# Performance work log

Hardware: AMD Instinct MI355X
Metric: run time of the kernel (lower is better)

The kernel has to match this reference:

```python
import jax, jax.numpy as jnp
import numpy as np

B, DIM_IN, T = 16, 512, 2048
DIM_OUT2 = 512 * 2  # dim_out * 2 (GLU halves it)
K = 3
STYLE = 128
SCALE_CONV = 1.0 / np.sqrt(DIM_IN * K ** 2).astype(np.float32)  # fan_in = dim_in * k^2 (as in source)
SCALE_LIN = 1.0 / np.sqrt(STYLE).astype(np.float32)


def setup_inputs() -> dict:
    key = jax.random.key(0)
    ks = jax.random.split(key, 6)
    x = jax.random.normal(ks[0], (B, DIM_IN, T), dtype=jnp.float32)
    c_src = jax.random.normal(ks[1], (B, STYLE), dtype=jnp.float32)
    c_trg = jax.random.normal(ks[2], (B, STYLE), dtype=jnp.float32)
    # EqualLinear params (lr_mul=1): weight ~ N(0,1), bias filled with bias_init=1
    w_s = jax.random.normal(ks[3], (DIM_IN, STYLE), dtype=jnp.float32)
    b_s = jnp.ones((DIM_IN,), dtype=jnp.float32)
    w_b = jax.random.normal(ks[4], (DIM_IN, STYLE), dtype=jnp.float32)
    b_b = jnp.ones((DIM_IN,), dtype=jnp.float32)
    weight = jax.random.normal(ks[5], (1, DIM_OUT2, DIM_IN, K), dtype=jnp.float32)
    return {"x": x, "c_src": c_src, "c_trg": c_trg,
            "w_s": w_s, "b_s": b_s, "w_b": w_b, "b_b": b_b, "weight": weight}


def reference(x, c_src, c_trg, w_s, b_s, w_b, b_b, weight):
    bsz, cin, t = x.shape
    cout = weight.shape[1]  # dim_out * 2
    k = weight.shape[3]
    # EqualLinear: F.linear(c, w*scale, bias)
    s = (c_trg @ (w_s * SCALE_LIN).T + b_s).reshape(bsz, 1, cin, 1)
    beta = (c_trg @ (w_b * SCALE_LIN).T + b_b).reshape(bsz, 1, cin, 1)
    w = SCALE_CONV * (weight * s + beta)               # [B, Cout, Cin, K]
    demod = jax.lax.rsqrt(jnp.sum(w * w, axis=(2, 3)) + 1e-8)   # [B, Cout]
    demod_mean = jnp.mean(w.reshape(bsz, cout, -1), axis=2)      # [B, Cout]
    w = (w - demod_mean[:, :, None, None]) * demod[:, :, None, None]
    # batch-as-groups conv1d
    w = w.reshape(bsz * cout, cin, k)
    xr = x.reshape(1, bsz * cin, t)
    out = jax.lax.conv_general_dilated(
        xr, w, window_strides=(1,), padding=[(k // 2, k // 2)],
        dimension_numbers=("NCH", "OIH", "NCH"), feature_group_count=bsz)
    out = out.reshape(bsz, cout, -1)
    a, g = jnp.split(out, 2, axis=1)  # GLU on channel dim
    return a * jax.nn.sigmoid(g)
```

## Files before the change

### kernel.cpp

```cpp
#include <hip/hip_runtime.h>
#include <math.h>

typedef __attribute__((ext_vector_type(8))) short short8;
typedef __attribute__((ext_vector_type(4))) float f32x4;
typedef unsigned short ushortT;

#define NB     16
#define CIN    512
#define TT     2048
#define COUT2  1024
#define NSTYLE 128
#define KKTOT  1536
#define TPAD   2050
#define NKT    24

#define SCALE_LIN  0.088388347648318447f
#define SCALE_CONV 0.014731391274719736f

__device__ __forceinline__ ushortT f2bf(float f) {
  union { float f; unsigned u; } v; v.f = f;
  unsigned r = v.u + 0x7fffu + ((v.u >> 16) & 1u);
  return (ushortT)(r >> 16);
}

__device__ __forceinline__ void gload16(const void* g, void* l) {
  __builtin_amdgcn_global_load_lds(
      (const __attribute__((address_space(1))) void*)g,
      (__attribute__((address_space(3))) void*)l, 16, 0, 0);
}

__global__ void style_kernel(const float* __restrict__ c_trg,
                             const float* __restrict__ w_s, const float* __restrict__ b_s,
                             const float* __restrict__ w_b, const float* __restrict__ b_b,
                             float* __restrict__ s, float* __restrict__ beta,
                             ushortT* __restrict__ xT) {
  int gid = blockIdx.x * 256 + threadIdx.x;
  int b = gid >> 9, ci = gid & 511;
  const float* ct = c_trg + b * NSTYLE;
  const float* ws = w_s + ci * NSTYLE;
  const float* wb = w_b + ci * NSTYLE;
  float as = 0.f, ab = 0.f;
#pragma unroll 8
  for (int j = 0; j < NSTYLE; ++j) {
    float c = ct[j];
    as += c * ws[j];
    ab += c * wb[j];
  }
  s[gid]    = as * SCALE_LIN + b_s[ci];
  beta[gid] = ab * SCALE_LIN + b_b[ci];
  xT[(size_t)b * TPAD * CIN + ci] = 0;
  xT[((size_t)b * TPAD + TPAD - 1) * CIN + ci] = 0;
}

__global__ void xpose_kernel(const float* __restrict__ x, ushortT* __restrict__ xT) {
  int b = blockIdx.z, ct = blockIdx.y, tt = blockIdx.x;
  int t0 = tt * 64, ci0 = ct * 64;
  __shared__ float tile[64][65];
  const float* xB = x + (size_t)b * CIN * TT;
  int rr = threadIdx.x >> 4;
  int c4 = threadIdx.x & 15;
#pragma unroll
  for (int it = 0; it < 4; ++it) {
    int ci = rr + it * 16;
    float4 v = *(const float4*)(xB + (size_t)(ci0 + ci) * TT + t0 + c4 * 4);
    tile[ci][c4 * 4 + 0] = v.x; tile[ci][c4 * 4 + 1] = v.y;
    tile[ci][c4 * 4 + 2] = v.z; tile[ci][c4 * 4 + 3] = v.w;
  }
  __syncthreads();
  ushortT* xTB = xT + (size_t)b * TPAD * CIN;
#pragma unroll
  for (int it = 0; it < 4; ++it) {
    int t = rr + it * 16;
    ushort4 o;
    o.x = f2bf(tile[c4 * 4 + 0][t]); o.y = f2bf(tile[c4 * 4 + 1][t]);
    o.z = f2bf(tile[c4 * 4 + 2][t]); o.w = f2bf(tile[c4 * 4 + 3][t]);
    *(ushort4*)(xTB + (size_t)(1 + t0 + t) * CIN + ci0 + c4 * 4) = o;
  }
}

__global__ void modw_kernel(const float* __restrict__ weight,
                            const float* __restrict__ s, const float* __restrict__ beta,
                            ushortT* __restrict__ wnorm) {
  int co = blockIdx.x, tid = threadIdx.x;
  int ci = tid * 2;
  const float* wp = weight + (size_t)co * KKTOT + (size_t)ci * 3;
  float2 va = *(const float2*)(wp);
  float2 vb = *(const float2*)(wp + 2);
  float2 vc = *(const float2*)(wp + 4);
  float v0 = va.x, v1 = va.y, v2 = vb.x, v3 = vb.y, v4 = vc.x, v5 = vc.y;
  int r = ((co & 511) << 1) | (co >> 9);
  __shared__ float rs[4], rq[4];
  for (int b = 0; b < NB; ++b) {
    float2 sv = *(const float2*)(s + b * CIN + ci);
    float2 ev = *(const float2*)(beta + b * CIN + ci);
    float w0 = SCALE_CONV * (v0 * sv.x + ev.x);
    float w1 = SCALE_CONV * (v1 * sv.x + ev.x);
    float w2 = SCALE_CONV * (v2 * sv.x + ev.x);
    float w3 = SCALE_CONV * (v3 * sv.y + ev.y);
    float w4 = SCALE_CONV * (v4 * sv.y + ev.y);
    float w5 = SCALE_CONV * (v5 * sv.y + ev.y);
    float sum = w0 + w1 + w2 + w3 + w4 + w5;
    float sq  = w0*w0 + w1*w1 + w2*w2 + w3*w3 + w4*w4 + w5*w5;
#pragma unroll
    for (int off = 32; off; off >>= 1) {
      sum += __shfl_xor(sum, off);
      sq  += __shfl_xor(sq,  off);
    }
    if ((tid & 63) == 0) { rs[tid >> 6] = sum; rq[tid >> 6] = sq; }
    __syncthreads();
    float mean  = (rs[0] + rs[1] + rs[2] + rs[3]) * (1.0f / 1536.0f);
    float demod = rsqrtf(rq[0] + rq[1] + rq[2] + rq[3] + 1e-8f);
    ushortT* dst = wnorm + ((size_t)b * COUT2 + r) * KKTOT;
    ushort2 p0, p1, p2;
    p0.x = f2bf((w0 - mean) * demod); p0.y = f2bf((w3 - mean) * demod);
    p1.x = f2bf((w1 - mean) * demod); p1.y = f2bf((w4 - mean) * demod);
    p2.x = f2bf((w2 - mean) * demod); p2.y = f2bf((w5 - mean) * demod);
    *(ushort2*)(dst +        ci) = p0;
    *(ushort2*)(dst +  512 + ci) = p1;
    *(ushort2*)(dst + 1024 + ci) = p2;
    __syncthreads();
  }
}


#define AFRAG(d, s, f) (*(const short8*)(ldsc + ((d) * 4 + (s)) * 16384 + aoff + (f) * 1024))
#define BFRAG(d, s, g) (*(const short8*)(ldsc + ((d) * 4 + 2 + (s)) * 16384 + boff + (g) * 1024))

#define RDA(as_, d, s, mh) do {              \
    as_##0 = AFRAG(d, s, (mh) * 4 + 0);      \
    as_##1 = AFRAG(d, s, (mh) * 4 + 1);      \
    as_##2 = AFRAG(d, s, (mh) * 4 + 2);      \
    as_##3 = AFRAG(d, s, (mh) * 4 + 3);      \
  } while (0)

#define RDB(bs_, d, s) do {                  \
    bs_##0 = BFRAG(d, s, 0);                 \
    bs_##1 = BFRAG(d, s, 1);                 \
    bs_##2 = BFRAG(d, s, 2);                 \
    bs_##3 = BFRAG(d, s, 3);                 \
  } while (0)

#define STAGE_A(d, s, kt) do {                                                   \
    int kc_ = (kt) * 64 + (s) * 32;                                              \
    gload16(wB + (size_t)(co0 + r0) * KKTOT + kc_ + jbs8,                        \
            ldsw + ((d) * 4 + (s)) * 8192 + tid * 8);                            \
    gload16(wB + (size_t)(co0 + r0 + 128) * KKTOT + kc_ + jbs8,                  \
            ldsw + ((d) * 4 + (s)) * 8192 + 4096 + tid * 8);                     \
  } while (0)

#define STAGE_B(d, s, kt) do {                                                   \
    int kc_ = (kt) * 64 + (s) * 32;                                              \
    int tap_ = kc_ >> 9; int ci_ = kc_ & 511;                                    \
    gload16(xB + (size_t)(t0 + r0 + tap_) * CIN + ci_ + jbs8,                    \
            ldsw + ((d) * 4 + 2 + (s)) * 8192 + tid * 8);                        \
    gload16(xB + (size_t)(t0 + r0 + 128 + tap_) * CIN + ci_ + jbs8,              \
            ldsw + ((d) * 4 + 2 + (s)) * 8192 + 4096 + tid * 8);                 \
  } while (0)

#define PHASE(mh, au_, bu_, RD_CODE, STAGES, VMN) do {                           \
    if ((VMN) == 6)      asm volatile("s_waitcnt vmcnt(6)" ::: "memory");        \
    else if ((VMN) == 4) asm volatile("s_waitcnt vmcnt(4)" ::: "memory");        \
    else if ((VMN) == 0) asm volatile("s_waitcnt vmcnt(0)" ::: "memory");        \
    __builtin_amdgcn_s_barrier();                                                \
    RD_CODE;                                                                     \
    STAGES;                                                                      \
    __builtin_amdgcn_s_setprio(1);                                               \
    acc[(mh)*4+0][0] = __builtin_amdgcn_mfma_f32_16x16x32_bf16(au_##0, bu_##0, acc[(mh)*4+0][0], 0, 0, 0); \
    acc[(mh)*4+0][1] = __builtin_amdgcn_mfma_f32_16x16x32_bf16(au_##0, bu_##1, acc[(mh)*4+0][1], 0, 0, 0); \
    acc[(mh)*4+0][2] = __builtin_amdgcn_mfma_f32_16x16x32_bf16(au_##0, bu_##2, acc[(mh)*4+0][2], 0, 0, 0); \
    acc[(mh)*4+0][3] = __builtin_amdgcn_mfma_f32_16x16x32_bf16(au_##0, bu_##3, acc[(mh)*4+0][3], 0, 0, 0); \
    acc[(mh)*4+1][0] = __builtin_amdgcn_mfma_f32_16x16x32_bf16(au_##1, bu_##0, acc[(mh)*4+1][0], 0, 0, 0); \
    acc[(mh)*4+1][1] = __builtin_amdgcn_mfma_f32_16x16x32_bf16(au_##1, bu_##1, acc[(mh)*4+1][1], 0, 0, 0); \
    acc[(mh)*4+1][2] = __builtin_amdgcn_mfma_f32_16x16x32_bf16(au_##1, bu_##2, acc[(mh)*4+1][2], 0, 0, 0); \
    acc[(mh)*4+1][3] = __builtin_amdgcn_mfma_f32_16x16x32_bf16(au_##1, bu_##3, acc[(mh)*4+1][3], 0, 0, 0); \
    acc[(mh)*4+2][0] = __builtin_amdgcn_mfma_f32_16x16x32_bf16(au_##2, bu_##0, acc[(mh)*4+2][0], 0, 0, 0); \
    acc[(mh)*4+2][1] = __builtin_amdgcn_mfma_f32_16x16x32_bf16(au_##2, bu_##1, acc[(mh)*4+2][1], 0, 0, 0); \
    acc[(mh)*4+2][2] = __builtin_amdgcn_mfma_f32_16x16x32_bf16(au_##2, bu_##2, acc[(mh)*4+2][2], 0, 0, 0); \
    acc[(mh)*4+2][3] = __builtin_amdgcn_mfma_f32_16x16x32_bf16(au_##2, bu_##3, acc[(mh)*4+2][3], 0, 0, 0); \
    acc[(mh)*4+3][0] = __builtin_amdgcn_mfma_f32_16x16x32_bf16(au_##3, bu_##0, acc[(mh)*4+3][0], 0, 0, 0); \
    acc[(mh)*4+3][1] = __builtin_amdgcn_mfma_f32_16x16x32_bf16(au_##3, bu_##1, acc[(mh)*4+3][1], 0, 0, 0); \
    acc[(mh)*4+3][2] = __builtin_amdgcn_mfma_f32_16x16x32_bf16(au_##3, bu_##2, acc[(mh)*4+3][2], 0, 0, 0); \
    acc[(mh)*4+3][3] = __builtin_amdgcn_mfma_f32_16x16x32_bf16(au_##3, bu_##3, acc[(mh)*4+3][3], 0, 0, 0); \
    __builtin_amdgcn_s_setprio(0);                                               \
  } while (0)

__global__ __launch_bounds__(512, 2)
void conv_gemm8(const ushortT* __restrict__ wnorm, const ushortT* __restrict__ xT,
                float* __restrict__ out) {
  extern __shared__ ushortT ldsw[];
  const char* ldsc = (const char*)ldsw;

  int orig = blockIdx.x;
  int wgid = (orig & 7) * 64 + (orig >> 3);
  int b  = wgid >> 5;
  int i5 = wgid & 31;
  int mp = i5 >> 4, r2 = i5 & 15;
  int nt = r2 >> 1, mt = mp * 2 + (r2 & 1);
  int co0 = mt * 256, t0 = nt * 256;

  int tid = threadIdx.x;
  int l = tid & 63, w = tid >> 6;
  int wm = w & 1, wn = w >> 1;

  int r0 = tid >> 2;
  int jbs8 = (((tid & 3) ^ ((r0 >> 1) & 3)) << 3);
  int cb = ((l >> 4) ^ ((l >> 1) & 3));
  int aoff = (wm * 128 + (l & 15)) * 64 + cb * 16;
  int boff = (wn * 64  + (l & 15)) * 64 + cb * 16;

  const ushortT* wB = wnorm + (size_t)b * COUT2 * KKTOT;
  const ushortT* xB = xT + (size_t)b * TPAD * CIN;

  f32x4 acc[8][4];
#pragma unroll
  for (int i = 0; i < 8; ++i)
#pragma unroll
    for (int j = 0; j < 4; ++j)
      acc[i][j] = (f32x4){0.f, 0.f, 0.f, 0.f};
  short8 ax0 = {}, ax1 = {}, ax2 = {}, ax3 = {};
  short8 ay0 = {}, ay1 = {}, ay2 = {}, ay3 = {};
  short8 bx0 = {}, bx1 = {}, bx2 = {}, bx3 = {};
  short8 by0 = {}, by1 = {}, by2 = {}, by3 = {};

  STAGE_A(0, 0, 0); STAGE_B(0, 0, 0); STAGE_A(0, 1, 0); STAGE_B(0, 1, 0);
  STAGE_B(1, 0, 1); STAGE_A(1, 0, 1); STAGE_B(1, 1, 1);
  asm volatile("s_waitcnt vmcnt(6)" ::: "memory");
  __builtin_amdgcn_s_barrier();
  RDA(ax, 0, 0, 0);
  RDB(bx, 0, 0);

  for (int j = 0; j < 11; ++j) {
    int kt1 = 2 * j + 1;
    int k0n = 2 * j + 2, k1n = 2 * j + 3;
    PHASE(0, ax, bx, { RDA(ay, 0, 0, 1); },                  STAGE_A(1, 1, kt1), -1);
    PHASE(1, ay, bx, { RDA(ax, 0, 1, 0); RDB(by, 0, 1); },   STAGE_B(0, 0, k0n), -1);
    PHASE(0, ax, by, { RDA(ay, 0, 1, 1); },                  STAGE_A(0, 0, k0n), -1);
    PHASE(1, ay, by, { RDA(ax, 1, 0, 0); RDB(bx, 1, 0); },   STAGE_B(0, 1, k0n),  4);
    PHASE(0, ax, bx, { RDA(ay, 1, 0, 1); },                  STAGE_A(0, 1, k0n), -1);
    PHASE(1, ay, bx, { RDA(ax, 1, 1, 0); RDB(by, 1, 1); },   STAGE_B(1, 0, k1n), -1);
    PHASE(0, ax, by, { RDA(ay, 1, 1, 1); },                  STAGE_A(1, 0, k1n), -1);
    PHASE(1, ay, by, { RDA(ax, 0, 0, 0); RDB(bx, 0, 0); },   STAGE_B(1, 1, k1n),  4);
  }
  PHASE(0, ax, bx, { RDA(ay, 0, 0, 1); },                  STAGE_A(1, 1, 23), -1);
  PHASE(1, ay, bx, { RDA(ax, 0, 1, 0); RDB(by, 0, 1); },   {},                -1);
  PHASE(0, ax, by, { RDA(ay, 0, 1, 1); },                  {},                -1);
  PHASE(1, ay, by, { RDA(ax, 1, 0, 0); RDB(bx, 1, 0); },   {},                 0);
  PHASE(0, ax, bx, { RDA(ay, 1, 0, 1); },                  {},                -1);
  PHASE(1, ay, bx, { RDA(ax, 1, 1, 0); RDB(by, 1, 1); },   {},                -1);
  PHASE(0, ax, by, { RDA(ay, 1, 1, 1); },                  {},                -1);
  PHASE(1, ay, by, { },                                    {},                -1);

#pragma unroll
  for (int f = 0; f < 8; ++f) {
    int cop = co0 + wm * 128 + f * 16 + ((l >> 4) << 2);
    int c = cop >> 1;
    size_t obase = ((size_t)b * (COUT2 / 2) + c) * TT;
#pragma unroll
    for (int g = 0; g < 4; ++g) {
      int t = t0 + wn * 64 + g * 16 + (l & 15);
      f32x4 v = acc[f][g];
      out[obase + t]      = v.x / (1.f + __expf(-v.y));
      out[obase + TT + t] = v.z / (1.f + __expf(-v.w));
    }
  }
}

extern "C" void kernel_launch(void* const* d_in, const int* in_sizes, int n_in,
                              void* d_out, int out_size, void* d_ws, size_t ws_size,
                              hipStream_t stream) {
  const float* x      = (const float*)d_in[0];
  const float* c_trg  = (const float*)d_in[2];
  const float* w_s    = (const float*)d_in[3];
  const float* b_s    = (const float*)d_in[4];
  const float* w_b    = (const float*)d_in[5];
  const float* b_b    = (const float*)d_in[6];
  const float* weight = (const float*)d_in[7];
  float* out = (float*)d_out;

  char* ws = (char*)d_ws;
  float*   s     = (float*)ws;
  float*   beta  = (float*)(ws + 32768);
  ushortT* xT    = (ushortT*)(ws + 65536);
  ushortT* wnorm = (ushortT*)(ws + 65536 + 33587200);

  hipFuncSetAttribute((const void*)conv_gemm8,
                      hipFuncAttributeMaxDynamicSharedMemorySize, 131072);

  style_kernel<<<32, 256, 0, stream>>>(c_trg, w_s, b_s, w_b, b_b, s, beta, xT);
  xpose_kernel<<<dim3(32, 8, 16), 256, 0, stream>>>(x, xT);
  modw_kernel<<<1024, 256, 0, stream>>>(weight, s, beta, wnorm);
  conv_gemm8<<<512, 512, 131072, stream>>>(wnorm, xT, out);
}
```

Before: 137.4 us.

## Halve barriers in conv GEMM pipeline, reorder stage issue, widen transpose stores

Restructures the main GEMM loop so a barrier and vmcnt wait happen only every other phase. Global-to-LDS stage loads are now issued before the LDS fragment reads, and the B-fragment offset is folded into boff. The transpose kernel now writes 8 bf16 values per 16-byte store instead of 4-wide stores. The goal is to cut barrier stalls and widen memory transactions, at the cost of a more fragile LDS hazard ordering that could race if the wait counts are wrong.

```diff
diff --git a/kernel.cpp b/kernel.cpp
--- a/kernel.cpp
+++ b/kernel.cpp
@@ -2,6 +2,7 @@
 #include <math.h>
 
 typedef __attribute__((ext_vector_type(8))) short short8;
+typedef __attribute__((ext_vector_type(8))) unsigned short ushort8;
 typedef __attribute__((ext_vector_type(4))) float f32x4;
 typedef unsigned short ushortT;
 
@@ -69,12 +70,14 @@
   __syncthreads();
   ushortT* xTB = xT + (size_t)b * TPAD * CIN;
 #pragma unroll
-  for (int it = 0; it < 4; ++it) {
-    int t = rr + it * 16;
-    ushort4 o;
-    o.x = f2bf(tile[c4 * 4 + 0][t]); o.y = f2bf(tile[c4 * 4 + 1][t]);
-    o.z = f2bf(tile[c4 * 4 + 2][t]); o.w = f2bf(tile[c4 * 4 + 3][t]);
-    *(ushort4*)(xTB + (size_t)(1 + t0 + t) * CIN + ci0 + c4 * 4) = o;
+  for (int it = 0; it < 2; ++it) {
+    int idx = it * 256 + threadIdx.x;
+    int c8 = idx & 7;
+    int tl = idx >> 3;
+    union { ushort8 v; ushortT u[8]; } o;
+#pragma unroll
+    for (int j = 0; j < 8; ++j) o.u[j] = f2bf(tile[c8 * 8 + j][tl]);
+    *(ushort8*)(xTB + (size_t)(1 + t0 + tl) * CIN + ci0 + c8 * 8) = o.v;
   }
 }
 
@@ -124,7 +127,7 @@
 
 
 #define AFRAG(d, s, f) (*(const short8*)(ldsc + ((d) * 4 + (s)) * 16384 + aoff + (f) * 1024))
-#define BFRAG(d, s, g) (*(const short8*)(ldsc + ((d) * 4 + 2 + (s)) * 16384 + boff + (g) * 1024))
+#define BFRAG(d, s, g) (*(const short8*)(ldsc + ((d) * 4 + (s)) * 16384 + boff + (g) * 1024))
 
 #define RDA(as_, d, s, mh) do {              \
     as_##0 = AFRAG(d, s, (mh) * 4 + 0);      \
@@ -157,13 +160,15 @@
             ldsw + ((d) * 4 + 2 + (s)) * 8192 + 4096 + tid * 8);                 \
   } while (0)
 
-#define PHASE(mh, au_, bu_, RD_CODE, STAGES, VMN) do {                           \
-    if ((VMN) == 6)      asm volatile("s_waitcnt vmcnt(6)" ::: "memory");        \
-    else if ((VMN) == 4) asm volatile("s_waitcnt vmcnt(4)" ::: "memory");        \
-    else if ((VMN) == 0) asm volatile("s_waitcnt vmcnt(0)" ::: "memory");        \
-    __builtin_amdgcn_s_barrier();                                                \
+#define PHASE(mh, au_, bu_, RD_CODE, STAGES, VMN, BAR) do {                      \
+    if (BAR) {                                                                   \
+      if ((VMN) == 6)      asm volatile("s_waitcnt vmcnt(6)" ::: "memory");      \
+      else if ((VMN) == 4) asm volatile("s_waitcnt vmcnt(4)" ::: "memory");      \
+      else if ((VMN) == 0) asm volatile("s_waitcnt vmcnt(0)" ::: "memory");      \
+      __builtin_amdgcn_s_barrier();                                              \
+    }                                                                            \
+    STAGES;                                                                      \
     RD_CODE;                                                                     \
-    STAGES;                                                                      \
     __builtin_amdgcn_s_setprio(1);                                               \
     acc[(mh)*4+0][0] = __builtin_amdgcn_mfma_f32_16x16x32_bf16(au_##0, bu_##0, acc[(mh)*4+0][0], 0, 0, 0); \
     acc[(mh)*4+0][1] = __builtin_amdgcn_mfma_f32_16x16x32_bf16(au_##0, bu_##1, acc[(mh)*4+0][1], 0, 0, 0); \
@@ -206,7 +211,7 @@
   int jbs8 = (((tid & 3) ^ ((r0 >> 1) & 3)) << 3);
   int cb = ((l >> 4) ^ ((l >> 1) & 3));
   int aoff = (wm * 128 + (l & 15)) * 64 + cb * 16;
-  int boff = (wn * 64  + (l & 15)) * 64 + cb * 16;
+  int boff = 32768 + (wn * 64 + (l & 15)) * 64 + cb * 16;
 
   const ushortT* wB = wnorm + (size_t)b * COUT2 * KKTOT;
   const ushortT* xB = xT + (size_t)b * TPAD * CIN;
@@ -232,23 +237,23 @@
   for (int j = 0; j < 11; ++j) {
     int kt1 = 2 * j + 1;
     int k0n = 2 * j + 2, k1n = 2 * j + 3;
-    PHASE(0, ax, bx, { RDA(ay, 0, 0, 1); },                  STAGE_A(1, 1, kt1), -1);
-    PHASE(1, ay, bx, { RDA(ax, 0, 1, 0); RDB(by, 0, 1); },   STAGE_B(0, 0, k0n), -1);
-    PHASE(0, ax, by, { RDA(ay, 0, 1, 1); },                  STAGE_A(0, 0, k0n), -1);
-    PHASE(1, ay, by, { RDA(ax, 1, 0, 0); RDB(bx, 1, 0); },   STAGE_B(0, 1, k0n),  4);
-    PHASE(0, ax, bx, { RDA(ay, 1, 0, 1); },                  STAGE_A(0, 1, k0n), -1);
-    PHASE(1, ay, bx, { RDA(ax, 1, 1, 0); RDB(by, 1, 1); },   STAGE_B(1, 0, k1n), -1);
-    PHASE(0, ax, by, { RDA(ay, 1, 1, 1); },                  STAGE_A(1, 0, k1n), -1);
-    PHASE(1, ay, by, { RDA(ax, 0, 0, 0); RDB(bx, 0, 0); },   STAGE_B(1, 1, k1n),  4);
-  }
-  PHASE(0, ax, bx, { RDA(ay, 0, 0, 1); },                  STAGE_A(1, 1, 23), -1);
-  PHASE(1, ay, bx, { RDA(ax, 0, 1, 0); RDB(by, 0, 1); },   {},                -1);
-  PHASE(0, ax, by, { RDA(ay, 0, 1, 1); },                  {},                -1);
-  PHASE(1, ay, by, { RDA(ax, 1, 0, 0); RDB(bx, 1, 0); },   {},                 0);
-  PHASE(0, ax, bx, { RDA(ay, 1, 0, 1); },                  {},                -1);
-  PHASE(1, ay, bx, { RDA(ax, 1, 1, 0); RDB(by, 1, 1); },   {},                -1);
-  PHASE(0, ax, by, { RDA(ay, 1, 1, 1); },                  {},                -1);
-  PHASE(1, ay, by, { },                                    {},                -1);
+    PHASE(0, ax, bx, { RDA(ay, 0, 0, 1); },                STAGE_A(1, 1, kt1),  6, 1);
+    PHASE(1, ay, bx, { RDA(ax, 0, 1, 0); RDB(by, 0, 1); }, STAGE_B(0, 0, k0n), -1, 0);
+    PHASE(0, ax, by, { RDA(ay, 0, 1, 1); },                STAGE_A(0, 0, k0n),  6, 1);
+    PHASE(1, ay, by, { RDA(ax, 1, 0, 0); RDB(bx, 1, 0); }, STAGE_B(0, 1, k0n), -1, 0);
+    PHASE(0, ax, bx, { RDA(ay, 1, 0, 1); },                STAGE_A(0, 1, k0n),  6, 1);
+    PHASE(1, ay, bx, { RDA(ax, 1, 1, 0); RDB(by, 1, 1); }, STAGE_B(1, 0, k1n), -1, 0);
+    PHASE(0, ax, by, { RDA(ay, 1, 1, 1); },                STAGE_A(1, 0, k1n),  6, 1);
+    PHASE(1, ay, by, { RDA(ax, 0, 0, 0); RDB(bx, 0, 0); }, STAGE_B(1, 1, k1n), -1, 0);
+  }
+  PHASE(0, ax, bx, { RDA(ay, 0, 0, 1); },                STAGE_A(1, 1, 23),  6, 1);
+  PHASE(1, ay, bx, { RDA(ax, 0, 1, 0); RDB(by, 0, 1); }, {},                -1, 0);
+  PHASE(0, ax, by, { RDA(ay, 0, 1, 1); },                {},                 4, 1);
+  PHASE(1, ay, by, { RDA(ax, 1, 0, 0); RDB(bx, 1, 0); }, {},                -1, 0);
+  PHASE(0, ax, bx, { RDA(ay, 1, 0, 1); },                {},                 0, 1);
+  PHASE(1, ay, bx, { RDA(ax, 1, 1, 0); RDB(by, 1, 1); }, {},                -1, 0);
+  PHASE(0, ax, by, { RDA(ay, 1, 1, 1); },                {},                -1, 1);
+  PHASE(1, ay, by, { },                                  {},                -1, 0);
 
 #pragma unroll
   for (int f = 0; f < 8; ++f) {
@@ -283,8 +288,8 @@
   ushortT* xT    = (ushortT*)(ws + 65536);
   ushortT* wnorm = (ushortT*)(ws + 65536 + 33587200);
 
-  hipFuncSetAttribute((const void*)conv_gemm8,
-                      hipFuncAttributeMaxDynamicSharedMemorySize, 131072);
+  (void)hipFuncSetAttribute((const void*)conv_gemm8,
+                            hipFuncAttributeMaxDynamicSharedMemorySize, 131072);
 
   style_kernel<<<32, 256, 0, stream>>>(c_trg, w_s, b_s, w_b, b_b, s, beta, xT);
   xpose_kernel<<<dim3(32, 8, 16), 256, 0, stream>>>(x, xT);
```

Result: no change. 136.3 us (-0.8%).
